# Kernel tuning notes

Measured on AMD Instinct MI355X. Metric: run time of the kernel, lower is better.

The kernel has to match this reference:

```python
import jax, jax.numpy as jnp
import numpy as np
import math

B_, S_, D_ = 8, 2048, 512
N_ = 16
EXPAND = 1.5
INNER = math.ceil(D_ * EXPAND)  # 768
K_ = 3
DELTA_MIN = 1e-4
DELTA_MAX = 3.0


def _hippo(n):
    A = np.zeros((n, n), np.float32)
    for i in range(n):
        ci = math.sqrt(2 * i + 1)
        for m in range(i + 1):
            cm = math.sqrt(2 * m + 1)
            if i == m:
                A[i, m] = -(2 * i + 1)
            else:
                A[i, m] = (-1.0 if (i - m) % 2 == 0 else 1.0) * ci * cm
    idx = np.arange(n, dtype=np.float32)
    Bv = np.sqrt(2.0 * idx + 1.0)
    Cv = Bv.copy()
    Cv[1::2] *= -1.0
    return A, Bv, Cv


def setup_inputs() -> dict:
    key = jax.random.key(0)
    k0, k1, k2, k3 = jax.random.split(key, 4)
    A0, Bv, Cv = _hippo(N_)
    scale = 1.0 / math.sqrt(INNER)
    return {
        "x": jax.random.normal(k0, (B_, S_, D_), jnp.float32),
        "ln_g": jnp.ones((D_,), jnp.float32),
        "ln_b": jnp.zeros((D_,), jnp.float32),
        "W_in": jax.random.normal(k1, (3 * INNER, D_), jnp.float32) / math.sqrt(D_),
        "conv_w": jax.random.normal(k2, (INNER, 1, K_), jnp.float32) / math.sqrt(K_),
        "A": jnp.asarray(A0),
        "Bmat": jnp.asarray(np.repeat(Bv[:, None], INNER, axis=1) * scale),  # (N, inner)
        "Cmat": jnp.asarray(np.repeat(Cv[None, :], INNER, axis=0) * scale),  # (inner, N)
        "W_out": jax.random.normal(k3, (D_, INNER), jnp.float32) / math.sqrt(INNER),
    }


def reference(x, ln_g, ln_b, W_in, conv_w, A, Bmat, Cmat, W_out):
    B, S, D = x.shape
    N = A.shape[0]
    # LayerNorm
    mu = jnp.mean(x, -1, keepdims=True)
    var = jnp.var(x, -1, keepdims=True)
    h = (x - mu) / jnp.sqrt(var + 1e-5) * ln_g + ln_b
    # Input projection -> data / gate / delta_raw
    proj = h @ W_in.T  # (B,S,3*inner)
    inner = proj.shape[-1] // 3
    data, gate, delta_raw = jnp.split(proj, 3, axis=-1)
    # Depthwise conv with padding K-1 then truncation to S == causal left pad K-1
    K = conv_w.shape[-1]
    dc = jax.lax.conv_general_dilated(
        data.transpose(0, 2, 1), conv_w, window_strides=(1,),
        padding=[(K - 1, 0)], dimension_numbers=("NCH", "OIH", "NCH"),
        feature_group_count=inner,
    ).transpose(0, 2, 1)  # (B,S,inner)
    u = jax.nn.silu(dc)
    # Data-dependent step size
    delta = jnp.mean(jax.nn.softplus(delta_raw), -1, keepdims=True) + DELTA_MIN
    delta = jnp.minimum(delta, DELTA_MAX)  # (B,S,1)
    # ZOH discretisation: A_disc = expm(delta*A); B_disc = A^{-1}(A_disc - I) B
    scaled_A = delta[..., None] * A  # (B,S,N,N)
    A_disc = jax.vmap(jax.scipy.linalg.expm)(scaled_A.reshape(-1, N, N)).reshape(B, S, N, N)
    rhs = A_disc - jnp.eye(N, dtype=x.dtype)
    integral = jnp.linalg.solve(jnp.broadcast_to(A, rhs.shape), rhs)  # (B,S,N,N)
    B_disc = integral @ Bmat  # (B,S,N,inner)

    def step(state, inputs):  # state: (B,N)
        Ad, Bd, ut = inputs  # (B,N,N), (B,N,inner), (B,inner)
        state = jnp.einsum("bnm,bm->bn", Ad, state) + jnp.einsum("bnd,bd->bn", Bd, ut)
        y = jnp.einsum("dn,bn->bd", Cmat, state)  # (B,inner)
        return state, y

    s0 = jnp.zeros((B, N), x.dtype)
    _, ys = jax.lax.scan(
        step, s0,
        (A_disc.transpose(1, 0, 2, 3), B_disc.transpose(1, 0, 2, 3), u.transpose(1, 0, 2)),
    )
    selective = ys.transpose(1, 0, 2)  # (B,S,inner)
    out = (jax.nn.sigmoid(gate) * selective) @ W_out.T
    return x + out
```

## Files before the change

kernel.cpp:

```cpp
#include <hip/hip_runtime.h>
#include <hip/hip_bf16.h>
#include <math.h>

#define BB 8
#define SS 2048
#define DD 512
#define II 768
#define MT (BB*SS)
#define NS 16
#define CH 32
#define NCB (SS/CH)
#define NCHK (MT/CH)
#define NT 1024

typedef __hip_bfloat16 bf16;
typedef __attribute__((ext_vector_type(8))) short bf16x8;
typedef __attribute__((ext_vector_type(4))) float f32x4;

__device__ __forceinline__ float fsigm(float x){
  return __builtin_amdgcn_rcpf(1.f + __expf(-x));
}
__device__ __forceinline__ float fsoftp(float x){
  return (x > 15.f) ? x : __logf(1.f + __expf(x));
}
__device__ __forceinline__ unsigned short f2bf_bits(float f){
  __hip_bfloat16 h = __float2bfloat16(f);
  return __builtin_bit_cast(unsigned short, h);
}
__device__ __forceinline__ float bfbits2f(short s){
  union { float f; unsigned u; } v;
  v.u = ((unsigned)(unsigned short)s) << 16;
  return v.f;
}
__device__ __forceinline__ void gload16(const bf16* src, void* dst){
  __builtin_amdgcn_global_load_lds((const __attribute__((address_space(1))) void*)src,
                                   (__attribute__((address_space(3))) void*)dst, 16, 0, 0);
}
__device__ __forceinline__ void gload16f(const float* src, void* dst){
  __builtin_amdgcn_global_load_lds((const __attribute__((address_space(1))) void*)src,
                                   (__attribute__((address_space(3))) void*)dst, 16, 0, 0);
}
template<int KDIM>
__device__ __forceinline__ bf16x8 lds_a_frag(const bf16* As, int row, int kseg){
  return *(const bf16x8*)((const char*)As + (size_t)row*(KDIM*2)
                          + (size_t)((kseg ^ (row & 7)) << 4));
}

__global__ __launch_bounds__(256) void cast_kernel(
    const float* __restrict__ in, bf16* __restrict__ out, int n4)
{
  int i = blockIdx.x*256 + threadIdx.x;
  if (i >= n4) return;
  float4 v = *(const float4*)&in[(size_t)i*4];
  ushort4 o = make_ushort4(f2bf_bits(v.x), f2bf_bits(v.y), f2bf_bits(v.z), f2bf_bits(v.w));
  *(ushort4*)&out[(size_t)i*4] = o;
}

__global__ __launch_bounds__(256) void bmsplit_kernel(
    const float* __restrict__ Bm, bf16* __restrict__ hi, bf16* __restrict__ lo)
{
  int i = blockIdx.x*256 + threadIdx.x;
  if (i >= NS*II) return;
  float f = Bm[i];
  unsigned short hb = f2bf_bits(f);
  hi[i] = __builtin_bit_cast(bf16, hb);
  lo[i] = __float2bfloat16(f - bfbits2f((short)hb));
}

__global__ __launch_bounds__(256) void apow_kernel(
    const float* __restrict__ A, float* __restrict__ Apow)
{
  __shared__ double Am[256], T0[256], T1[256];
  __shared__ double colsum[16];
  int tid = threadIdx.x, r = tid>>4, c = tid&15;
  double a = (double)A[tid];
  Am[tid] = a; T0[tid] = a;
  Apow[tid] = A[tid];
  __syncthreads();
  double *Tc = T0, *Tn = T1;
  for (int k=2;k<=13;k++){
    double s = 0.0;
    #pragma unroll
    for (int j=0;j<16;j++) s += Tc[r*16+j]*Am[j*16+c];
    Tn[tid] = s;
    Apow[(k-1)*256 + tid] = (float)s;
    __syncthreads();
    double* tmp = Tc; Tc = Tn; Tn = tmp;
  }
  if (tid < 16){
    double s = 0.0;
    #pragma unroll
    for (int j=0;j<16;j++) s += fabs(Am[j*16+tid]);
    colsum[tid] = s;
  }
  __syncthreads();
  if (tid == 0){
    double mx = 0.0;
    #pragma unroll
    for (int j=0;j<16;j++) mx = fmax(mx, colsum[j]);
    Apow[13*256] = (float)mx;
  }
}

__global__ __launch_bounds__(64) void etab_kernel(
    const float* __restrict__ Apow, float* __restrict__ Etab,
    float* __restrict__ Gtab, float* __restrict__ dEtab)
{
  int i = blockIdx.x;
  int l = threadIdx.x;
  int r = l&15, gq = l>>4, c0 = gq*4;
  __shared__ alignas(16) float bufE[256];
  __shared__ alignas(16) float bufG[256];
  float delta = (3.0f*i)/(float)(NT-1);
  float anorm = Apow[13*256];
  float mx = delta*anorm;
  int s = 0;
  if (mx > 2.f){
    s = (int)ceilf(log2f(mx)) - 1;
    if (s < 0) s = 0;
    if (s > 12) s = 12;
  }
  float dsc = ldexpf(delta, -s);
  const float invk[14]  = {0.f, 1.f, 0.5f, 1.f/3.f, 0.25f, 0.2f, 1.f/6.f, 1.f/7.f,
                           0.125f, 1.f/9.f, 0.1f, 1.f/11.f, 1.f/12.f, 1.f/13.f};
  float4 e = make_float4(0.f,0.f,0.f,0.f), g = e;
  if (r==c0  ){ e.x = 1.f; g.x = dsc; }
  if (r==c0+1){ e.y = 1.f; g.y = dsc; }
  if (r==c0+2){ e.z = 1.f; g.z = dsc; }
  if (r==c0+3){ e.w = 1.f; g.w = dsc; }
  float ck = 1.f;
  #pragma unroll
  for (int k=1;k<=13;k++){
    ck *= dsc * invk[k];
    float gk = ck * dsc / (float)(k+1);
    float4 ap = *(const float4*)&Apow[(k-1)*256 + r*16 + c0];
    e.x = fmaf(ck, ap.x, e.x); e.y = fmaf(ck, ap.y, e.y);
    e.z = fmaf(ck, ap.z, e.z); e.w = fmaf(ck, ap.w, e.w);
    g.x = fmaf(gk, ap.x, g.x); g.y = fmaf(gk, ap.y, g.y);
    g.z = fmaf(gk, ap.z, g.z); g.w = fmaf(gk, ap.w, g.w);
  }
  for (int it=0; it<s; ++it){
    *(float4*)&bufE[r*16+c0] = e;
    *(float4*)&bufG[r*16+c0] = g;
    __syncthreads();
    float erow[16];
    #pragma unroll
    for (int q4=0;q4<4;q4++){
      float4 tv = *(const float4*)&bufE[r*16+q4*4];
      erow[q4*4+0]=tv.x; erow[q4*4+1]=tv.y; erow[q4*4+2]=tv.z; erow[q4*4+3]=tv.w;
    }
    float4 en = make_float4(0.f,0.f,0.f,0.f);
    float4 gn = g;
    #pragma unroll
    for (int kk=0;kk<16;kk++){
      float4 ev = *(const float4*)&bufE[kk*16+c0];
      float4 gv = *(const float4*)&bufG[kk*16+c0];
      float ek = erow[kk];
      en.x=fmaf(ek,ev.x,en.x); en.y=fmaf(ek,ev.y,en.y);
      en.z=fmaf(ek,ev.z,en.z); en.w=fmaf(ek,ev.w,en.w);
      gn.x=fmaf(ek,gv.x,gn.x); gn.y=fmaf(ek,gv.y,gn.y);
      gn.z=fmaf(ek,gv.z,gn.z); gn.w=fmaf(ek,gv.w,gn.w);
    }
    e = en; g = gn;
    __syncthreads();
  }
  size_t o = (size_t)i*256 + r*16 + c0;
  *(float4*)&Etab[o] = e;
  *(float4*)&Gtab[o] = g;
  *(float4*)&bufE[r*16+c0] = e;
  __syncthreads();
  float4 de = make_float4(0.f,0.f,0.f,0.f);
  #pragma unroll
  for (int q4=0;q4<4;q4++){
    float4 ar = *(const float4*)&Apow[r*16 + q4*4];
    float4 e0 = *(const float4*)&bufE[(q4*4+0)*16 + c0];
    float4 e1 = *(const float4*)&bufE[(q4*4+1)*16 + c0];
    float4 e2 = *(const float4*)&bufE[(q4*4+2)*16 + c0];
    float4 e3 = *(const float4*)&bufE[(q4*4+3)*16 + c0];
    de.x = fmaf(ar.x,e0.x,fmaf(ar.y,e1.x,fmaf(ar.z,e2.x,fmaf(ar.w,e3.x,de.x))));
    de.y = fmaf(ar.x,e0.y,fmaf(ar.y,e1.y,fmaf(ar.z,e2.y,fmaf(ar.w,e3.y,de.y))));
    de.z = fmaf(ar.x,e0.z,fmaf(ar.y,e1.z,fmaf(ar.z,e2.z,fmaf(ar.w,e3.z,de.z))));
    de.w = fmaf(ar.x,e0.w,fmaf(ar.y,e1.w,fmaf(ar.z,e2.w,fmaf(ar.w,e3.w,de.w))));
  }
  *(float4*)&dEtab[o] = de;
}

__global__ __launch_bounds__(256) void ln_kernel(
    const float* __restrict__ x, const float* __restrict__ g,
    const float* __restrict__ b, bf16* __restrict__ h)
{
  int w = threadIdx.x >> 6, l = threadIdx.x & 63;
  int m = blockIdx.x*4 + w;
  const float* xr = x + (size_t)m*DD;
  float4 v0 = *(const float4*)&xr[l*4];
  float4 v1 = *(const float4*)&xr[256 + l*4];
  float s  = v0.x+v0.y+v0.z+v0.w + v1.x+v1.y+v1.z+v1.w;
  float sq = v0.x*v0.x+v0.y*v0.y+v0.z*v0.z+v0.w*v0.w
           + v1.x*v1.x+v1.y*v1.y+v1.z*v1.z+v1.w*v1.w;
  #pragma unroll
  for (int o=1;o<64;o<<=1){ s += __shfl_xor(s,o); sq += __shfl_xor(sq,o); }
  float mu  = s*(1.f/DD);
  float var = sq*(1.f/DD) - mu*mu;
  float rs  = rsqrtf(var + 1e-5f);
  float4 g0 = *(const float4*)&g[l*4];
  float4 b0 = *(const float4*)&b[l*4];
  float4 g1 = *(const float4*)&g[256 + l*4];
  float4 b1 = *(const float4*)&b[256 + l*4];
  ushort4 o0, o1;
  o0.x = f2bf_bits((v0.x-mu)*rs*g0.x + b0.x);
  o0.y = f2bf_bits((v0.y-mu)*rs*g0.y + b0.y);
  o0.z = f2bf_bits((v0.z-mu)*rs*g0.z + b0.z);
  o0.w = f2bf_bits((v0.w-mu)*rs*g0.w + b0.w);
  o1.x = f2bf_bits((v1.x-mu)*rs*g1.x + b1.x);
  o1.y = f2bf_bits((v1.y-mu)*rs*g1.y + b1.y);
  o1.z = f2bf_bits((v1.z-mu)*rs*g1.z + b1.z);
  o1.w = f2bf_bits((v1.w-mu)*rs*g1.w + b1.w);
  *(ushort4*)&h[(size_t)m*DD + l*4]       = o0;
  *(ushort4*)&h[(size_t)m*DD + 256 + l*4] = o1;
}


__global__ __launch_bounds__(256, 3) void gemm1_mfma(
    const bf16* __restrict__ Ah, const bf16* __restrict__ Bw,
    bf16* __restrict__ databf, bf16* __restrict__ gatebf, float* __restrict__ dacc)
{
  __shared__ alignas(16) bf16 As[128*64];
  __shared__ alignas(16) bf16 Bs[128*64];
  const int tid = threadIdx.x, l = tid & 63, w = tid >> 6;
  const int lrow = l & 15, lgrp = l >> 4;
  const int orig = blockIdx.x;
  const int swz = (orig & 7) * (2304/8) + (orig >> 3);
  const int bm = (swz / 18) * 128;
  const int bn = swz % 18;
  const int wrow = (w >> 1) * 64, wcol = (w & 1) * 64;

  f32x4 acc[4][4];
  #pragma unroll
  for (int i=0;i<4;i++){
    #pragma unroll
    for (int f=0;f<4;f++){ f32x4 z={0.f,0.f,0.f,0.f}; acc[i][f]=z; }
  }

  for (int t=0; t<8; ++t){
    #pragma unroll
    for (int it=0; it<4; ++it){
      int d = tid + it*256;
      int r = d >> 3, s = d & 7;
      gload16(Ah + (size_t)(bm + r)*DD + t*64 + ((s ^ (r&7))<<3),
              (char*)As + (size_t)(d - l)*16);
    }
    #pragma unroll
    for (int it=0; it<4; ++it){
      int d = tid + it*256;
      int r = d >> 3, s = d & 7;
      gload16(Bw + (size_t)(bn*128 + r)*DD + t*64 + ((s ^ (r&7))<<3),
              (char*)Bs + (size_t)(d - l)*16);
    }
    __syncthreads();
    #pragma unroll
    for (int kk=0; kk<2; ++kk){
      bf16x8 afr[4], bfr[4];
      #pragma unroll
      for (int i=0;i<4;i++) afr[i] = lds_a_frag<64>(As, wrow + i*16 + lrow, kk*4 + lgrp);
      #pragma unroll
      for (int f=0;f<4;f++) bfr[f] = lds_a_frag<64>(Bs, wcol + f*16 + lrow, kk*4 + lgrp);
      #pragma unroll
      for (int i=0;i<4;i++){
        #pragma unroll
        for (int f=0;f<4;f++)
          acc[i][f] = __builtin_amdgcn_mfma_f32_16x16x32_bf16(afr[i], bfr[f], acc[i][f], 0,0,0);
      }
    }
    __syncthreads();
  }

  const int rowb = bm + wrow + lgrp*4;
  const int cglob = bn*128 + wcol + lrow;
  if (bn < 6){
    #pragma unroll
    for (int i=0;i<4;i++){
      #pragma unroll
      for (int f=0;f<4;f++){
        int col = cglob + f*16;
        #pragma unroll
        for (int j=0;j<4;j++)
          databf[(size_t)(rowb + i*16 + j)*II + col] = __float2bfloat16(acc[i][f][j]);
      }
    }
  } else if (bn < 12){
    #pragma unroll
    for (int i=0;i<4;i++){
      #pragma unroll
      for (int f=0;f<4;f++){
        int col = cglob - 768 + f*16;
        #pragma unroll
        for (int j=0;j<4;j++)
          gatebf[(size_t)(rowb + i*16 + j)*II + col] = __float2bfloat16(fsigm(acc[i][f][j]));
      }
    }
  } else {
    #pragma unroll
    for (int i=0;i<4;i++){
      #pragma unroll
      for (int j=0;j<4;j++){
        float v = fsoftp(acc[i][0][j]) + fsoftp(acc[i][1][j])
                + fsoftp(acc[i][2][j]) + fsoftp(acc[i][3][j]);
        v += __shfl_xor(v,1); v += __shfl_xor(v,2);
        v += __shfl_xor(v,4); v += __shfl_xor(v,8);
        if (lrow == 0) atomicAdd(&dacc[rowb + i*16 + j], v);
      }
    }
  }
}

__global__ __launch_bounds__(256, 3) void gemm2_mfma(
    const bf16* __restrict__ Asel, const bf16* __restrict__ Bw,
    const float* __restrict__ x, float* __restrict__ out)
{
  __shared__ alignas(16) bf16 As[128*64];
  __shared__ alignas(16) bf16 Bs[128*64];
  const int tid = threadIdx.x, l = tid & 63, w = tid >> 6;
  const int lrow = l & 15, lgrp = l >> 4;
  const int orig = blockIdx.x;
  const int swz = (orig & 7) * (512/8) + (orig >> 3);
  const int bm = (swz >> 2) * 128;
  const int bn = swz & 3;
  const int wrow = (w >> 1) * 64, wcol = (w & 1) * 64;

  f32x4 acc[4][4];
  #pragma unroll
  for (int i=0;i<4;i++){
    #pragma unroll
    for (int f=0;f<4;f++){ f32x4 z={0.f,0.f,0.f,0.f}; acc[i][f]=z; }
  }

  for (int t=0; t<12; ++t){
    #pragma unroll
    for (int it=0; it<4; ++it){
      int d = tid + it*256;
      int r = d >> 3, s = d & 7;
      gload16(Asel + (size_t)(bm + r)*II + t*64 + ((s ^ (r&7))<<3),
              (char*)As + (size_t)(d - l)*16);
    }
    #pragma unroll
    for (int it=0; it<4; ++it){
      int d = tid + it*256;
      int r = d >> 3, s = d & 7;
      gload16(Bw + (size_t)(bn*128 + r)*II + t*64 + ((s ^ (r&7))<<3),
              (char*)Bs + (size_t)(d - l)*16);
    }
    __syncthreads();
    #pragma unroll
    for (int kk=0; kk<2; ++kk){
      bf16x8 afr[4], bfr[4];
      #pragma unroll
      for (int i=0;i<4;i++) afr[i] = lds_a_frag<64>(As, wrow + i*16 + lrow, kk*4 + lgrp);
      #pragma unroll
      for (int f=0;f<4;f++) bfr[f] = lds_a_frag<64>(Bs, wcol + f*16 + lrow, kk*4 + lgrp);
      #pragma unroll
      for (int i=0;i<4;i++){
        #pragma unroll
        for (int f=0;f<4;f++)
          acc[i][f] = __builtin_amdgcn_mfma_f32_16x16x32_bf16(afr[i], bfr[f], acc[i][f], 0,0,0);
      }
    }
    __syncthreads();
  }

  const int rowb = bm + wrow + lgrp*4;
  #pragma unroll
  for (int i=0;i<4;i++){
    #pragma unroll
    for (int f=0;f<4;f++){
      int col = bn*128 + wcol + f*16 + lrow;
      #pragma unroll
      for (int j=0;j<4;j++){
        size_t e = (size_t)(rowb + i*16 + j)*DD + col;
        out[e] = acc[i][f][j] + x[e];
      }
    }
  }
}

__global__ __launch_bounds__(256) void convw_mfma(
    const bf16* __restrict__ data, const float* __restrict__ cw,
    const bf16* __restrict__ Bmhi, const bf16* __restrict__ Bmlo,
    float* __restrict__ w_all)
{
  const int tid = threadIdx.x, l = tid & 63, wv = tid >> 6;
  const int lrow = l & 15, lgrp = l >> 4;
  const int p0 = blockIdx.x * 16;
  const int p  = p0 + lrow;
  const int t  = p & (SS-1);
  const float mask1 = (t>=1) ? 1.f : 0.f;
  const float mask0 = (t>=2) ? 1.f : 0.f;
  const int r1 = (t>=1) ? p-1 : p;
  const int r0 = (t>=2) ? p-2 : p;
  const int cbase = wv*192 + lgrp*8;
  const bf16* dp2 = data + (size_t)p *II + cbase;
  const bf16* dp1 = data + (size_t)r1*II + cbase;
  const bf16* dp0 = data + (size_t)r0*II + cbase;
  const bf16* bh  = Bmhi + lrow*II + cbase;
  const bf16* bl  = Bmlo + lrow*II + cbase;
  const float* cwp = cw + 3*cbase;

  f32x4 acc = {0.f,0.f,0.f,0.f};
  #pragma unroll
  for (int u=0; u<6; ++u){
    const int c0 = u*32;
    bf16x8 v2 = *(const bf16x8*)(dp2 + c0);
    bf16x8 v1 = *(const bf16x8*)(dp1 + c0);
    bf16x8 v0 = *(const bf16x8*)(dp0 + c0);
    bf16x8 ah = *(const bf16x8*)(bh + c0);
    bf16x8 al = *(const bf16x8*)(bl + c0);
    float cv[24];
    #pragma unroll
    for (int q=0;q<6;q++){
      float4 cq = *(const float4*)(cwp + u*96 + q*4);
      cv[q*4+0]=cq.x; cv[q*4+1]=cq.y; cv[q*4+2]=cq.z; cv[q*4+3]=cq.w;
    }
    bf16x8 Bh, Bl;
    #pragma unroll
    for (int j=0;j<8;j++){
      float d2 = bfbits2f(v2[j]);
      float d1 = bfbits2f(v1[j]) * mask1;
      float d0 = bfbits2f(v0[j]) * mask0;
      float a = fmaf(d0, cv[3*j], fmaf(d1, cv[3*j+1], d2*cv[3*j+2]));
      float u2 = a * fsigm(a);
      unsigned short hb = f2bf_bits(u2);
      Bh[j] = (short)hb;
      Bl[j] = (short)f2bf_bits(u2 - bfbits2f((short)hb));
    }
    acc = __builtin_amdgcn_mfma_f32_16x16x32_bf16(ah, Bh, acc, 0,0,0);
    acc = __builtin_amdgcn_mfma_f32_16x16x32_bf16(ah, Bl, acc, 0,0,0);
    acc = __builtin_amdgcn_mfma_f32_16x16x32_bf16(al, Bh, acc, 0,0,0);
  }
  __shared__ alignas(16) float red[4][64*4];
  *(f32x4*)&red[wv][l*4] = acc;
  __syncthreads();
  if (wv == 0){
    f32x4 s0 = *(const f32x4*)&red[0][l*4];
    f32x4 s1 = *(const f32x4*)&red[1][l*4];
    f32x4 s2 = *(const f32x4*)&red[2][l*4];
    f32x4 s3 = *(const f32x4*)&red[3][l*4];
    f32x4 s = s0 + s1 + s2 + s3;
    *(f32x4*)&w_all[(size_t)p*NS + lgrp*4] = s;
  }
}

__global__ __launch_bounds__(256) void scan1_kernel(
    const float* __restrict__ Etab, const float* __restrict__ Gtab,
    const float* __restrict__ dEtab, const float* __restrict__ dacc,
    const float* __restrict__ w_all,
    float* __restrict__ Ad, float* __restrict__ c_all,
    float* __restrict__ P, float* __restrict__ q)
{
  int cc = blockIdx.x;
  int bb = cc / NCB, ci = cc % NCB;
  size_t base = (size_t)bb*SS + (size_t)ci*CH;
  int tid = threadIdx.x;
  int i = tid>>4, j = tid&15;
  __shared__ float Pb[2][256];
  __shared__ float qb[2][16];
  __shared__ float AdS[256];
  Pb[0][tid] = (i==j)?1.f:0.f;
  if (tid<16) qb[0][tid]=0.f;
  int cur = 0;
  const float hh = 3.f/(float)(NT-1);
  for (int t=0;t<CH;t++){
    size_t m = base + t;
    float delta = fminf(dacc[m]*(1.f/II) + 1e-4f, 3.0f);
    float tf = delta * (float)(NT-1) * (1.f/3.f);
    int i0 = (int)tf;
    if (i0 > NT-2) i0 = NT-2;
    float fr = tf - (float)i0;
    float fr2 = fr*fr, fr3 = fr2*fr;
    float h00 = 2.f*fr3 - 3.f*fr2 + 1.f;
    float h10 = fr3 - 2.f*fr2 + fr;
    float h01 = -2.f*fr3 + 3.f*fr2;
    float h11 = fr3 - fr2;
    size_t o0 = (size_t)i0*256 + tid;
    float E0 = Etab[o0], E1 = Etab[o0+256];
    float D0 = dEtab[o0], D1 = dEtab[o0+256];
    float G0 = Gtab[o0], G1 = Gtab[o0+256];
    float e = h00*E0 + h01*E1 + hh*(h10*D0 + h11*D1);
    float g = h00*G0 + h01*G1 + hh*(h10*E0 + h11*E1);
    Ad[m*256 + tid] = e;
    float cv = g * w_all[m*NS + j];
    cv += __shfl_xor(cv,1); cv += __shfl_xor(cv,2);
    cv += __shfl_xor(cv,4); cv += __shfl_xor(cv,8);
    if (j==0) c_all[m*NS + i] = cv;
    AdS[tid] = e;
    __syncthreads();
    float acc = 0.f;
    #pragma unroll
    for (int k=0;k<16;k++) acc = fmaf(AdS[i*16+k], Pb[cur][k*16+j], acc);
    float qa = 0.f;
    if (j==0){
      #pragma unroll
      for (int k=0;k<16;k++) qa = fmaf(AdS[i*16+k], qb[cur][k], qa);
      qa += cv;
    }
    __syncthreads();
    Pb[cur^1][tid] = acc;
    if (j==0) qb[cur^1][i] = qa;
    cur ^= 1;
  }
  __syncthreads();
  P[(size_t)cc*256 + tid] = Pb[cur][tid];
  if (tid<16) q[(size_t)cc*NS + tid] = qb[cur][tid];
}

__global__ __launch_bounds__(64) void scan2_kernel(
    const float* __restrict__ P, const float* __restrict__ q,
    float* __restrict__ entry)
{
  int b = blockIdx.x;
  int l = threadIdx.x;
  __shared__ alignas(16) float Pl[2][256];
  __shared__ float el[2][16];
  if (l < 16) el[0][l] = 0.f;
  gload16f(P + (size_t)(b*NCB)*256 + l*4, (char*)Pl[0]);
  float qv = q[(size_t)(b*NCB)*NS + (l & 15)];
  int cur = 0;
  for (int ci=0; ci<NCB; ci++){
    __syncthreads();
    int cc = b*NCB + ci;
    if (ci+1 < NCB)
      gload16f(P + (size_t)(cc+1)*256 + l*4, (char*)Pl[cur^1]);
    float qn = (ci+1 < NCB) ? q[(size_t)(cc+1)*NS + (l&15)] : 0.f;
    if (l < 16){
      entry[(size_t)cc*NS + l] = el[cur][l];
      float a = qv;
      #pragma unroll
      for (int k=0;k<16;k++) a = fmaf(Pl[cur][l*16+k], el[cur][k], a);
      el[cur^1][l] = a;
    }
    qv = qn;
    cur ^= 1;
  }
}

__global__ __launch_bounds__(256) void scan3sel_kernel(
    const float* __restrict__ Ad, const float* __restrict__ c_all,
    const float* __restrict__ entry, const float* __restrict__ Cm,
    const bf16* __restrict__ gate, bf16* __restrict__ selg)
{
  int cc = blockIdx.x;
  int bb = cc / NCB, ci = cc % NCB;
  size_t base = (size_t)bb*SS + (size_t)ci*CH;
  int tid = threadIdx.x, l = tid & 63, w = tid >> 6;
  int r = l & 15;
  float g[16];
  #pragma unroll
  for (int k=0;k<16;k++) g[k] = entry[(size_t)cc*NS + k];
  for (int t=0;t<CH;t++){
    size_t m = base + t;
    const float* Er = &Ad[m*256 + r*16];
    float s = c_all[m*NS + r];
    #pragma unroll
    for (int q4=0;q4<4;q4++){
      float4 ev = *(const float4*)&Er[q4*4];
      s = fmaf(ev.x, g[q4*4+0], s);
      s = fmaf(ev.y, g[q4*4+1], s);
      s = fmaf(ev.z, g[q4*4+2], s);
      s = fmaf(ev.w, g[q4*4+3], s);
    }
    #pragma unroll
    for (int k=0;k<16;k++) g[k] = __shfl(s, k);
    #pragma unroll
    for (int p=0;p<3;p++){
      int jcol = w*192 + p*64 + l;
      float y = 0.f;
      #pragma unroll
      for (int q4=0;q4<4;q4++){
        float4 cv = *(const float4*)&Cm[jcol*16 + q4*4];
        y = fmaf(cv.x, g[q4*4+0], y);
        y = fmaf(cv.y, g[q4*4+1], y);
        y = fmaf(cv.z, g[q4*4+2], y);
        y = fmaf(cv.w, g[q4*4+3], y);
      }
      size_t e = m*II + jcol;
      float gv = __bfloat162float(gate[e]);
      selg[e] = __float2bfloat16(gv*y);
    }
  }
}

extern "C" void kernel_launch(void* const* d_in, const int* in_sizes, int n_in,
                              void* d_out, int out_size, void* d_ws, size_t ws_size,
                              hipStream_t stream) {
  (void)in_sizes; (void)n_in; (void)out_size; (void)ws_size;
  const float* x      = (const float*)d_in[0];
  const float* ln_g   = (const float*)d_in[1];
  const float* ln_b   = (const float*)d_in[2];
  const float* W_in   = (const float*)d_in[3];
  const float* conv_w = (const float*)d_in[4];
  const float* A      = (const float*)d_in[5];
  const float* Bm     = (const float*)d_in[6];
  const float* Cm     = (const float*)d_in[7];
  const float* Wout   = (const float*)d_in[8];
  float* out = (float*)d_out;

  char* ws = (char*)d_ws;
  size_t off = 0;
  #define WSALLOC(ty, name, count) \
    ty* name = (ty*)(ws + off); off += (((size_t)(count))*sizeof(ty) + 255) & ~(size_t)255;
  WSALLOC(bf16,  hbf,    (size_t)MT*DD)
  WSALLOC(bf16,  databf, (size_t)MT*II)
  WSALLOC(bf16,  gatebf, (size_t)MT*II)
  WSALLOC(float, dacc,   MT)
  WSALLOC(float, w_all,  (size_t)MT*NS)
  WSALLOC(float, Ad,     (size_t)MT*256)
  WSALLOC(float, c_all,  (size_t)MT*NS)
  WSALLOC(float, Pbuf,   (size_t)NCHK*256)
  WSALLOC(float, qbuf,   (size_t)NCHK*NS)
  WSALLOC(float, entry,  (size_t)NCHK*NS)
  WSALLOC(bf16,  Winbf,  (size_t)3*II*DD)
  WSALLOC(bf16,  Woutbf, (size_t)DD*II)
  WSALLOC(bf16,  Bmhi,   (size_t)NS*II)
  WSALLOC(bf16,  Bmlo,   (size_t)NS*II)
  WSALLOC(float, Apow,   13*256 + 16)
  WSALLOC(float, Etab,   (size_t)NT*256)
  WSALLOC(float, Gtab,   (size_t)NT*256)
  WSALLOC(float, dEtab,  (size_t)NT*256)
  #undef WSALLOC

  hipMemsetAsync(dacc, 0, (size_t)MT*sizeof(float), stream);
  cast_kernel  <<<(3*II*DD/4 + 255)/256, 256, 0, stream>>>(W_in,  Winbf,  3*II*DD/4);
  cast_kernel  <<<(DD*II/4   + 255)/256, 256, 0, stream>>>(Wout,  Woutbf, DD*II/4);
  bmsplit_kernel<<<(NS*II + 255)/256, 256, 0, stream>>>(Bm, Bmhi, Bmlo);
  apow_kernel  <<<1, 256, 0, stream>>>(A, Apow);
  etab_kernel  <<<NT, 64, 0, stream>>>(Apow, Etab, Gtab, dEtab);
  ln_kernel    <<<MT/4, 256, 0, stream>>>(x, ln_g, ln_b, hbf);
  gemm1_mfma   <<<dim3(2304), 256, 0, stream>>>(hbf, Winbf, databf, gatebf, dacc);
  convw_mfma   <<<MT/16, 256, 0, stream>>>(databf, conv_w, Bmhi, Bmlo, w_all);
  scan1_kernel <<<NCHK, 256, 0, stream>>>(Etab, Gtab, dEtab, dacc, w_all, Ad, c_all, Pbuf, qbuf);
  scan2_kernel <<<BB, 64, 0, stream>>>(Pbuf, qbuf, entry);
  scan3sel_kernel<<<NCHK, 256, 0, stream>>>(Ad, c_all, entry, Cm, gatebf, databf);
  gemm2_mfma   <<<dim3(512), 256, 0, stream>>>(databf, Woutbf, x, out);
}
```

Measured before the change: 231.5 us.

## Double-buffer LDS in both GEMMs and stage conv inputs through shared memory

Both MFMA GEMM kernels now use two LDS buffers, so the global loads for the next K-tile are issued while the current tile is computed. This halves the barriers per tile, and launch bounds drop from 3 to 2 blocks per CU to fit the doubled shared memory. The conv-weight kernel now loads the 18-row data window and the conv weights into LDS once per block instead of reading three overlapping rows per thread from global memory. The costs are lower occupancy in the GEMMs and extra LDS traffic and a barrier in the conv kernel.

```diff
diff --git a/kernel.cpp b/kernel.cpp
--- a/kernel.cpp
+++ b/kernel.cpp
@@ -220,12 +220,12 @@
 }
 
 
-__global__ __launch_bounds__(256, 3) void gemm1_mfma(
+__global__ __launch_bounds__(256, 2) void gemm1_mfma(
     const bf16* __restrict__ Ah, const bf16* __restrict__ Bw,
     bf16* __restrict__ databf, bf16* __restrict__ gatebf, float* __restrict__ dacc)
 {
-  __shared__ alignas(16) bf16 As[128*64];
-  __shared__ alignas(16) bf16 Bs[128*64];
+  __shared__ alignas(16) bf16 As0[128*64], Bs0[128*64];
+  __shared__ alignas(16) bf16 As1[128*64], Bs1[128*64];
   const int tid = threadIdx.x, l = tid & 63, w = tid >> 6;
   const int lrow = l & 15, lgrp = l >> 4;
   const int orig = blockIdx.x;
@@ -241,29 +241,30 @@
     for (int f=0;f<4;f++){ f32x4 z={0.f,0.f,0.f,0.f}; acc[i][f]=z; }
   }
 
-  for (int t=0; t<8; ++t){
+  auto stage = [&](int t, bf16* Asb, bf16* Bsb){
     #pragma unroll
     for (int it=0; it<4; ++it){
       int d = tid + it*256;
       int r = d >> 3, s = d & 7;
       gload16(Ah + (size_t)(bm + r)*DD + t*64 + ((s ^ (r&7))<<3),
-              (char*)As + (size_t)(d - l)*16);
+              (char*)Asb + (size_t)(d - l)*16);
     }
     #pragma unroll
     for (int it=0; it<4; ++it){
       int d = tid + it*256;
       int r = d >> 3, s = d & 7;
       gload16(Bw + (size_t)(bn*128 + r)*DD + t*64 + ((s ^ (r&7))<<3),
-              (char*)Bs + (size_t)(d - l)*16);
-    }
-    __syncthreads();
+              (char*)Bsb + (size_t)(d - l)*16);
+    }
+  };
+  auto compute = [&](const bf16* Asb, const bf16* Bsb){
     #pragma unroll
     for (int kk=0; kk<2; ++kk){
       bf16x8 afr[4], bfr[4];
       #pragma unroll
-      for (int i=0;i<4;i++) afr[i] = lds_a_frag<64>(As, wrow + i*16 + lrow, kk*4 + lgrp);
-      #pragma unroll
-      for (int f=0;f<4;f++) bfr[f] = lds_a_frag<64>(Bs, wcol + f*16 + lrow, kk*4 + lgrp);
+      for (int i=0;i<4;i++) afr[i] = lds_a_frag<64>(Asb, wrow + i*16 + lrow, kk*4 + lgrp);
+      #pragma unroll
+      for (int f=0;f<4;f++) bfr[f] = lds_a_frag<64>(Bsb, wcol + f*16 + lrow, kk*4 + lgrp);
       #pragma unroll
       for (int i=0;i<4;i++){
         #pragma unroll
@@ -271,6 +272,17 @@
           acc[i][f] = __builtin_amdgcn_mfma_f32_16x16x32_bf16(afr[i], bfr[f], acc[i][f], 0,0,0);
       }
     }
+  };
+
+  stage(0, As0, Bs0);
+  __syncthreads();
+  #pragma unroll 1
+  for (int tt=0; tt<4; ++tt){
+    stage(2*tt+1, As1, Bs1);
+    compute(As0, Bs0);
+    __syncthreads();
+    if (tt < 3) stage(2*tt+2, As0, Bs0);
+    compute(As1, Bs1);
     __syncthreads();
   }
 
@@ -313,12 +325,12 @@
   }
 }
 
-__global__ __launch_bounds__(256, 3) void gemm2_mfma(
+__global__ __launch_bounds__(256, 2) void gemm2_mfma(
     const bf16* __restrict__ Asel, const bf16* __restrict__ Bw,
     const float* __restrict__ x, float* __restrict__ out)
 {
-  __shared__ alignas(16) bf16 As[128*64];
-  __shared__ alignas(16) bf16 Bs[128*64];
+  __shared__ alignas(16) bf16 As0[128*64], Bs0[128*64];
+  __shared__ alignas(16) bf16 As1[128*64], Bs1[128*64];
   const int tid = threadIdx.x, l = tid & 63, w = tid >> 6;
   const int lrow = l & 15, lgrp = l >> 4;
   const int orig = blockIdx.x;
@@ -334,29 +346,30 @@
     for (int f=0;f<4;f++){ f32x4 z={0.f,0.f,0.f,0.f}; acc[i][f]=z; }
   }
 
-  for (int t=0; t<12; ++t){
+  auto stage = [&](int t, bf16* Asb, bf16* Bsb){
     #pragma unroll
     for (int it=0; it<4; ++it){
       int d = tid + it*256;
       int r = d >> 3, s = d & 7;
       gload16(Asel + (size_t)(bm + r)*II + t*64 + ((s ^ (r&7))<<3),
-              (char*)As + (size_t)(d - l)*16);
+              (char*)Asb + (size_t)(d - l)*16);
     }
     #pragma unroll
     for (int it=0; it<4; ++it){
       int d = tid + it*256;
       int r = d >> 3, s = d & 7;
       gload16(Bw + (size_t)(bn*128 + r)*II + t*64 + ((s ^ (r&7))<<3),
-              (char*)Bs + (size_t)(d - l)*16);
-    }
-    __syncthreads();
+              (char*)Bsb + (size_t)(d - l)*16);
+    }
+  };
+  auto compute = [&](const bf16* Asb, const bf16* Bsb){
     #pragma unroll
     for (int kk=0; kk<2; ++kk){
       bf16x8 afr[4], bfr[4];
       #pragma unroll
-      for (int i=0;i<4;i++) afr[i] = lds_a_frag<64>(As, wrow + i*16 + lrow, kk*4 + lgrp);
-      #pragma unroll
-      for (int f=0;f<4;f++) bfr[f] = lds_a_frag<64>(Bs, wcol + f*16 + lrow, kk*4 + lgrp);
+      for (int i=0;i<4;i++) afr[i] = lds_a_frag<64>(Asb, wrow + i*16 + lrow, kk*4 + lgrp);
+      #pragma unroll
+      for (int f=0;f<4;f++) bfr[f] = lds_a_frag<64>(Bsb, wcol + f*16 + lrow, kk*4 + lgrp);
       #pragma unroll
       for (int i=0;i<4;i++){
         #pragma unroll
@@ -364,6 +377,17 @@
           acc[i][f] = __builtin_amdgcn_mfma_f32_16x16x32_bf16(afr[i], bfr[f], acc[i][f], 0,0,0);
       }
     }
+  };
+
+  stage(0, As0, Bs0);
+  __syncthreads();
+  #pragma unroll 1
+  for (int tt=0; tt<6; ++tt){
+    stage(2*tt+1, As1, Bs1);
+    compute(As0, Bs0);
+    __syncthreads();
+    if (tt < 5) stage(2*tt+2, As0, Bs0);
+    compute(As1, Bs1);
     __syncthreads();
   }
 
@@ -387,32 +411,49 @@
     const bf16* __restrict__ Bmhi, const bf16* __restrict__ Bmlo,
     float* __restrict__ w_all)
 {
+  __shared__ alignas(16) bf16  Ds[1728*8];
+  __shared__ alignas(16) float cwl[II*3];
+  __shared__ alignas(16) float red[4][256];
   const int tid = threadIdx.x, l = tid & 63, wv = tid >> 6;
   const int lrow = l & 15, lgrp = l >> 4;
   const int p0 = blockIdx.x * 16;
   const int p  = p0 + lrow;
   const int t  = p & (SS-1);
+  const int bstart = p0 & ~(SS-1);
   const float mask1 = (t>=1) ? 1.f : 0.f;
   const float mask0 = (t>=2) ? 1.f : 0.f;
-  const int r1 = (t>=1) ? p-1 : p;
-  const int r0 = (t>=2) ? p-2 : p;
-  const int cbase = wv*192 + lgrp*8;
-  const bf16* dp2 = data + (size_t)p *II + cbase;
-  const bf16* dp1 = data + (size_t)r1*II + cbase;
-  const bf16* dp0 = data + (size_t)r0*II + cbase;
-  const bf16* bh  = Bmhi + lrow*II + cbase;
-  const bf16* bl  = Bmlo + lrow*II + cbase;
-  const float* cwp = cw + 3*cbase;
+
+  #pragma unroll
+  for (int it=0; it<7; ++it){
+    int d = tid + it*256;
+    if (d < 1728){
+      int r = d % 18, s2 = d / 18;
+      int prow = p0 - 2 + r; if (prow < bstart) prow = bstart;
+      gload16(data + (size_t)prow*II + s2*8, (char*)Ds + (size_t)(d - l)*16);
+    }
+  }
+  #pragma unroll
+  for (int it=0; it<3; ++it){
+    int d = tid + it*256;
+    if (d < 576)
+      gload16f(cw + d*4, (char*)cwl + (size_t)(d - l)*16);
+  }
+  __syncthreads();
+
+  const int sB = wv*24 + lgrp;
+  const char* DsB = (const char*)Ds + ((size_t)sB*18 + lrow)*16;
+  const bf16* bh  = Bmhi + (size_t)lrow*II + sB*8;
+  const bf16* bl  = Bmlo + (size_t)lrow*II + sB*8;
+  const float* cwp = cwl + sB*24;
 
   f32x4 acc = {0.f,0.f,0.f,0.f};
   #pragma unroll
   for (int u=0; u<6; ++u){
-    const int c0 = u*32;
-    bf16x8 v2 = *(const bf16x8*)(dp2 + c0);
-    bf16x8 v1 = *(const bf16x8*)(dp1 + c0);
-    bf16x8 v0 = *(const bf16x8*)(dp0 + c0);
-    bf16x8 ah = *(const bf16x8*)(bh + c0);
-    bf16x8 al = *(const bf16x8*)(bl + c0);
+    bf16x8 v0 = *(const bf16x8*)(DsB + (size_t)u*72*16);
+    bf16x8 v1 = *(const bf16x8*)(DsB + (size_t)u*72*16 + 16);
+    bf16x8 v2 = *(const bf16x8*)(DsB + (size_t)u*72*16 + 32);
+    bf16x8 ah = *(const bf16x8*)(bh + u*32);
+    bf16x8 al = *(const bf16x8*)(bl + u*32);
     float cv[24];
     #pragma unroll
     for (int q=0;q<6;q++){
@@ -435,7 +476,6 @@
     acc = __builtin_amdgcn_mfma_f32_16x16x32_bf16(ah, Bl, acc, 0,0,0);
     acc = __builtin_amdgcn_mfma_f32_16x16x32_bf16(al, Bh, acc, 0,0,0);
   }
-  __shared__ alignas(16) float red[4][64*4];
   *(f32x4*)&red[wv][l*4] = acc;
   __syncthreads();
   if (wv == 0){
```

New measurement: 222.9 us. 1.04x faster.

## Stage conv, scan1 and scan3 operands in LDS to cut global latency

Applied to the files above, without the earlier changes.

convw_mfma now loads each block's 18-row data window and the conv weights into shared memory with async 16-byte loads, instead of re-reading three overlapping rows from global memory per lane. scan1 first computes all 32 interpolated transition matrices into shared memory, then runs the sequential product with one barrier per step instead of two. scan3sel prefetches the chunk's Ad matrices (with an XOR swizzle) and c values into shared memory before the serial loop. The aim is to shorten latency-bound serial loops and remove redundant global reads, at the cost of much larger LDS use per block and therefore possibly lower occupancy.

```diff
diff --git a/kernel.cpp b/kernel.cpp
--- a/kernel.cpp
+++ b/kernel.cpp
@@ -387,32 +387,49 @@
     const bf16* __restrict__ Bmhi, const bf16* __restrict__ Bmlo,
     float* __restrict__ w_all)
 {
+  __shared__ alignas(16) bf16  Ds[1728*8];
+  __shared__ alignas(16) float cwl[II*3];
+  __shared__ alignas(16) float red[4][256];
   const int tid = threadIdx.x, l = tid & 63, wv = tid >> 6;
   const int lrow = l & 15, lgrp = l >> 4;
   const int p0 = blockIdx.x * 16;
   const int p  = p0 + lrow;
   const int t  = p & (SS-1);
+  const int bstart = p0 & ~(SS-1);
   const float mask1 = (t>=1) ? 1.f : 0.f;
   const float mask0 = (t>=2) ? 1.f : 0.f;
-  const int r1 = (t>=1) ? p-1 : p;
-  const int r0 = (t>=2) ? p-2 : p;
-  const int cbase = wv*192 + lgrp*8;
-  const bf16* dp2 = data + (size_t)p *II + cbase;
-  const bf16* dp1 = data + (size_t)r1*II + cbase;
-  const bf16* dp0 = data + (size_t)r0*II + cbase;
-  const bf16* bh  = Bmhi + lrow*II + cbase;
-  const bf16* bl  = Bmlo + lrow*II + cbase;
-  const float* cwp = cw + 3*cbase;
+
+  #pragma unroll
+  for (int it=0; it<7; ++it){
+    int d = tid + it*256;
+    if (d < 1728){
+      int r = d % 18, s2 = d / 18;
+      int prow = p0 - 2 + r; if (prow < bstart) prow = bstart;
+      gload16(data + (size_t)prow*II + s2*8, (char*)Ds + (size_t)(d - l)*16);
+    }
+  }
+  #pragma unroll
+  for (int it=0; it<3; ++it){
+    int d = tid + it*256;
+    if (d < 576)
+      gload16f(cw + d*4, (char*)cwl + (size_t)(d - l)*16);
+  }
+  __syncthreads();
+
+  const int sB = wv*24 + lgrp;
+  const char* DsB = (const char*)Ds + ((size_t)sB*18 + lrow)*16;
+  const bf16* bh  = Bmhi + (size_t)lrow*II + sB*8;
+  const bf16* bl  = Bmlo + (size_t)lrow*II + sB*8;
+  const float* cwp = cwl + sB*24;
 
   f32x4 acc = {0.f,0.f,0.f,0.f};
   #pragma unroll
   for (int u=0; u<6; ++u){
-    const int c0 = u*32;
-    bf16x8 v2 = *(const bf16x8*)(dp2 + c0);
-    bf16x8 v1 = *(const bf16x8*)(dp1 + c0);
-    bf16x8 v0 = *(const bf16x8*)(dp0 + c0);
-    bf16x8 ah = *(const bf16x8*)(bh + c0);
-    bf16x8 al = *(const bf16x8*)(bl + c0);
+    bf16x8 v0 = *(const bf16x8*)(DsB + (size_t)u*72*16);
+    bf16x8 v1 = *(const bf16x8*)(DsB + (size_t)u*72*16 + 16);
+    bf16x8 v2 = *(const bf16x8*)(DsB + (size_t)u*72*16 + 32);
+    bf16x8 ah = *(const bf16x8*)(bh + u*32);
+    bf16x8 al = *(const bf16x8*)(bl + u*32);
     float cv[24];
     #pragma unroll
     for (int q=0;q<6;q++){
@@ -435,7 +452,6 @@
     acc = __builtin_amdgcn_mfma_f32_16x16x32_bf16(ah, Bl, acc, 0,0,0);
     acc = __builtin_amdgcn_mfma_f32_16x16x32_bf16(al, Bh, acc, 0,0,0);
   }
-  __shared__ alignas(16) float red[4][64*4];
   *(f32x4*)&red[wv][l*4] = acc;
   __syncthreads();
   if (wv == 0){
@@ -460,12 +476,12 @@
   size_t base = (size_t)bb*SS + (size_t)ci*CH;
   int tid = threadIdx.x;
   int i = tid>>4, j = tid&15;
+  __shared__ float Et[CH][256];
+  __shared__ float cb[CH][16];
   __shared__ float Pb[2][256];
   __shared__ float qb[2][16];
-  __shared__ float AdS[256];
   Pb[0][tid] = (i==j)?1.f:0.f;
   if (tid<16) qb[0][tid]=0.f;
-  int cur = 0;
   const float hh = 3.f/(float)(NT-1);
   for (int t=0;t<CH;t++){
     size_t m = base + t;
@@ -486,27 +502,29 @@
     float e = h00*E0 + h01*E1 + hh*(h10*D0 + h11*D1);
     float g = h00*G0 + h01*G1 + hh*(h10*E0 + h11*E1);
     Ad[m*256 + tid] = e;
+    Et[t][j*16 + i] = e;
     float cv = g * w_all[m*NS + j];
     cv += __shfl_xor(cv,1); cv += __shfl_xor(cv,2);
     cv += __shfl_xor(cv,4); cv += __shfl_xor(cv,8);
-    if (j==0) c_all[m*NS + i] = cv;
-    AdS[tid] = e;
-    __syncthreads();
-    float acc = 0.f;
-    #pragma unroll
-    for (int k=0;k<16;k++) acc = fmaf(AdS[i*16+k], Pb[cur][k*16+j], acc);
+    if (j==0){ c_all[m*NS + i] = cv; cb[t][i] = cv; }
+  }
+  __syncthreads();
+  int cur = 0;
+  for (int t=0;t<CH;t++){
+    float acc2 = 0.f;
+    #pragma unroll
+    for (int k=0;k<16;k++) acc2 = fmaf(Et[t][k*16+i], Pb[cur][k*16+j], acc2);
     float qa = 0.f;
     if (j==0){
       #pragma unroll
-      for (int k=0;k<16;k++) qa = fmaf(AdS[i*16+k], qb[cur][k], qa);
-      qa += cv;
-    }
-    __syncthreads();
-    Pb[cur^1][tid] = acc;
+      for (int k=0;k<16;k++) qa = fmaf(Et[t][k*16+i], qb[cur][k], qa);
+      qa += cb[t][i];
+    }
+    Pb[cur^1][tid] = acc2;
     if (j==0) qb[cur^1][i] = qa;
+    __syncthreads();
     cur ^= 1;
   }
-  __syncthreads();
   P[(size_t)cc*256 + tid] = Pb[cur][tid];
   if (tid<16) q[(size_t)cc*NS + tid] = qb[cur][tid];
 }
@@ -546,21 +564,38 @@
     const float* __restrict__ entry, const float* __restrict__ Cm,
     const bf16* __restrict__ gate, bf16* __restrict__ selg)
 {
+  __shared__ alignas(16) float Ads[CH*256];
+  __shared__ alignas(16) float cl[CH*16];
   int cc = blockIdx.x;
   int bb = cc / NCB, ci = cc % NCB;
   size_t base = (size_t)bb*SS + (size_t)ci*CH;
   int tid = threadIdx.x, l = tid & 63, w = tid >> 6;
   int r = l & 15;
+  const float* Adc = Ad + base*256;
+  #pragma unroll
+  for (int it=0; it<8; ++it){
+    int d = tid + it*256;
+    int tt = d >> 6, rr = (d >> 2) & 15, k4 = d & 3;
+    gload16f(Adc + tt*256 + rr*16 + ((k4 ^ ((rr>>1)&3))<<2),
+             (char*)Ads + (size_t)(d - l)*16);
+  }
+  {
+    int d = tid;
+    if (d < 128)
+      gload16f(c_all + base*NS + d*4, (char*)cl + (size_t)(d - l)*16);
+  }
   float g[16];
   #pragma unroll
   for (int k=0;k<16;k++) g[k] = entry[(size_t)cc*NS + k];
+  __syncthreads();
+
+  const int frm = (r>>1)&3;
   for (int t=0;t<CH;t++){
     size_t m = base + t;
-    const float* Er = &Ad[m*256 + r*16];
-    float s = c_all[m*NS + r];
+    float s = cl[t*16 + r];
     #pragma unroll
     for (int q4=0;q4<4;q4++){
-      float4 ev = *(const float4*)&Er[q4*4];
+      float4 ev = *(const float4*)&Ads[(t*64 + r*4 + (q4 ^ frm))*4];
       s = fmaf(ev.x, g[q4*4+0], s);
       s = fmaf(ev.y, g[q4*4+1], s);
       s = fmaf(ev.z, g[q4*4+2], s);
```

Result: faster. 206.9 us (-10.6%).
